# Kernel tuning notes

Measured on AMD Instinct MI355X. Metric: run time of the kernel, lower is better.

Reference implementation:

```python
import jax, jax.numpy as jnp
import numpy as np

PATCH_SIZE = 32          # BinaryPatchCompressor default
MAX_ACTIVE = 512         # memory_size // 2
EPS = 1e-8               # torch F.cosine_similarity eps


def _compress(emb, base):
    # emb, base: [S, D]. Entropy-ranked top-k row selection + int8 truncation.
    diff = emb - base
    entropy = jnp.std(diff, axis=-1, ddof=1)                  # [S] (torch std is unbiased)
    k = min(PATCH_SIZE, entropy.shape[0])
    _, idx = jax.lax.top_k(entropy, k)
    idx = jnp.sort(idx)
    # patch.to(torch.int8): truncation toward zero (values assumed in int8 range)
    patch = jnp.trunc(jnp.clip(diff[idx], -128.0, 127.0))     # [k, D]
    return patch, idx


def _decompress(patch, base, idx):
    # reconstructed[indices] += patch  -> scatter-add
    return base.at[idx].add(patch)


def _meta_embed(feats, W1, b1, W2, b2):
    # meta_learner: Linear(D+3,128) -> ReLU -> Linear(128,D)
    return jax.nn.relu(feats @ W1 + b1) @ W2 + b2


def setup_inputs() -> dict:
    key = jax.random.key(0)
    ks = jax.random.split(key, 6)
    S, D, N = 2048, 1024, 32
    return {
        "query": jax.random.normal(ks[0], (S, D), jnp.float32),
        "memories": jax.random.normal(ks[1], (N, S, D), jnp.float32),
        "surprise": jax.random.uniform(ks[2], (N,), jnp.float32),
        "priority_mult": jax.random.uniform(ks[3], (N,), jnp.float32) + 0.5,
        "W1": jax.random.normal(ks[4], (D + 3, 128), jnp.float32) * 0.02,
        "b1": jnp.zeros((128,), jnp.float32),
        "W2": jax.random.normal(ks[5], (128, D), jnp.float32) * 0.02,
        "b2": jnp.zeros((D,), jnp.float32),
    }


def reference(query, memories, surprise, priority_mult, W1, b1, W2, b2):
    S, D = query.shape
    N = memories.shape[0]
    base = jnp.zeros_like(query)                              # [S, D]

    # per-memory entropy-topk compression (vectorized over N)
    patches, idxs = jax.vmap(lambda m: _compress(m, base))(memories)      # [N,k,D], [N,k]
    # scatter-add decompression
    decompressed = jax.vmap(lambda p, i: _decompress(p, base, i))(patches, idxs)  # [N,S,D]

    # ApiAdapter aggregation: cat(query, decompressed).mean over memory axis
    src = jnp.concatenate([query[None], decompressed], axis=0)           # [N+1,S,D]
    aggregated = src.mean(axis=0)                                        # [S,D]

    # compress the aggregate, then reconstruct via scatter-add
    out_patch, out_idx = _compress(aggregated, base)
    recon = _decompress(out_patch, base, out_idx)                        # [S,D]

    # MemScheduler: meta-learned embeddings + priority-weighted cosine sims
    mem_feats = jnp.concatenate(
        [memories.mean(axis=1), surprise[:, None], jnp.zeros((N, 2), query.dtype)], axis=1)
    mem_emb = _meta_embed(mem_feats, W1, b1, W2, b2)                     # [N,D]
    q_feat = jnp.concatenate([query.mean(axis=0), jnp.zeros((3,), query.dtype)])
    q_emb = _meta_embed(q_feat, W1, b1, W2, b2)                          # [D]

    sims = (mem_emb @ q_emb) / (
        jnp.maximum(jnp.linalg.norm(mem_emb, axis=-1), EPS)
        * jnp.maximum(jnp.linalg.norm(q_emb), EPS))
    sims = sims * priority_mult                                          # [N]
    _, top_idx = jax.lax.top_k(sims, min(N, MAX_ACTIVE))
    return recon, sims, top_idx
```

## Files before the change

kernel.cpp:

```cpp
#include <hip/hip_runtime.h>
#include <math.h>

#define S     2048
#define D     1024
#define NMEM  32
#define KP    32

__device__ inline float trunc_clip(float v) {
    return truncf(fminf(fmaxf(v, -128.f), 127.f));
}

__global__ __launch_bounds__(256)
void k_stats(const float* __restrict__ mem, const float* __restrict__ query,
             float* __restrict__ entropy, float* __restrict__ colsumPart) {
    const int tid = threadIdx.x, wave = tid >> 6, lane = tid & 63;
    const int n    = blockIdx.x >> 5;
    const int tile = blockIdx.x & 31;
    const float* src = (n < NMEM) ? (mem + (size_t)n * S * D) : query;
    const int s0 = tile * 64 + wave * 16;

    __shared__ double redsm[64][33];
    __shared__ double redsq[64][33];
    __shared__ float  ldscol[D];
    for (int i = tid; i < D; i += 256) ldscol[i] = 0.f;
    __syncthreads();

    float colacc[16];
    #pragma unroll
    for (int i = 0; i < 16; ++i) colacc[i] = 0.f;

    for (int r = 0; r < 16; ++r) {
        const float4* row = (const float4*)(src + (size_t)(s0 + r) * D);
        double sm = 0.0, sq = 0.0;
        #pragma unroll
        for (int it = 0; it < 4; ++it) {
            float4 v = row[it * 64 + lane];
            sm += (double)v.x + (double)v.y + (double)v.z + (double)v.w;
            sq += (double)v.x * v.x + (double)v.y * v.y
                + (double)v.z * v.z + (double)v.w * v.w;
            colacc[it*4+0] += v.x; colacc[it*4+1] += v.y;
            colacc[it*4+2] += v.z; colacc[it*4+3] += v.w;
        }
        sm += __shfl_xor(sm, 1, 64);
        sq += __shfl_xor(sq, 1, 64);
        if ((lane & 1) == 0) {
            redsm[wave * 16 + r][lane >> 1] = sm;
            redsq[wave * 16 + r][lane >> 1] = sq;
        }
    }
    #pragma unroll
    for (int it = 0; it < 4; ++it)
        #pragma unroll
        for (int j = 0; j < 4; ++j)
            atomicAdd(&ldscol[it*256 + lane*4 + j], colacc[it*4+j]);
    __syncthreads();

    if (n < NMEM) {
        const int row = tid >> 2, qq = tid & 3;
        double sm = 0.0, sq = 0.0;
        #pragma unroll
        for (int i = 0; i < 8; ++i) { sm += redsm[row][qq*8 + i]; sq += redsq[row][qq*8 + i]; }
        sm += __shfl_xor(sm, 1, 64); sq += __shfl_xor(sq, 1, 64);
        sm += __shfl_xor(sm, 2, 64); sq += __shfl_xor(sq, 2, 64);
        if (qq == 0) {
            double var = (sq - sm * sm / (double)D) / (double)(D - 1);
            entropy[(size_t)n * S + tile * 64 + row] = (float)sqrt(var > 0.0 ? var : 0.0);
        }
    }
    for (int i = tid; i < D; i += 256)
        colsumPart[((size_t)n * 32 + tile) * D + i] = ldscol[i];
}

__global__ __launch_bounds__(1024)
void k_select(const float* __restrict__ entropy, const float* __restrict__ colsumPart,
              int* __restrict__ idxSel, float* __restrict__ feats) {
    const int n = blockIdx.x, tid = threadIdx.x;
    {
        float acc = 0.f;
        #pragma unroll 4
        for (int t = 0; t < 32; ++t) acc += colsumPart[((size_t)n * 32 + t) * D + tid];
        feats[(size_t)n * D + tid] = acc * (1.f / (float)S);
    }
    if (n >= NMEM) return;

    __shared__ unsigned long long key[S];
    const float* e = entropy + (size_t)n * S;
    for (int i = tid; i < S; i += 1024) {
        unsigned int b = __float_as_uint(e[i]);
        key[i] = ((unsigned long long)b << 32) | (unsigned long long)(S - 1 - i);
    }
    __syncthreads();
    const unsigned long long k0 = key[tid], k1 = key[tid + 1024];
    int c0 = 0, c1 = 0;
    for (int j = 0; j < S; j += 4) {
        unsigned long long a0 = key[j], a1 = key[j+1], a2 = key[j+2], a3 = key[j+3];
        c0 += (a0 > k0) + (a1 > k0) + (a2 > k0) + (a3 > k0);
        c1 += (a0 > k1) + (a1 > k1) + (a2 > k1) + (a3 > k1);
    }
    if (c0 < KP) idxSel[n * KP + c0] = tid;
    if (c1 < KP) idxSel[n * KP + c1] = tid + 1024;
}

__global__ __launch_bounds__(256)
void k_aggregate(const float* __restrict__ mem, const float* __restrict__ query,
                 const int* __restrict__ idxSel, float* __restrict__ agg,
                 float* __restrict__ entAgg) {
    const int s = blockIdx.x, tid = threadIdx.x;
    __shared__ int    sidx[NMEM * KP];
    __shared__ int    sel_n[NMEM];
    __shared__ int    selCount;
    __shared__ double rsm[256], rsq[256];
    __shared__ double fsm[64],  fsq[64];
    if (tid == 0) selCount = 0;
    for (int i = tid; i < NMEM * KP; i += 256) sidx[i] = idxSel[i];
    __syncthreads();
    #pragma unroll
    for (int k = 0; k < 4; ++k) {
        int e = tid * 4 + k;
        if (sidx[e] == s) { int p = atomicAdd(&selCount, 1); sel_n[p] = e >> 5; }
    }
    __syncthreads();

    float4 acc = ((const float4*)(query + (size_t)s * D))[tid];
    const int cnt = selCount;
    for (int c = 0; c < cnt; ++c) {
        const int n = sel_n[c];
        float4 v = ((const float4*)(mem + ((size_t)n * S + s) * D))[tid];
        acc.x += trunc_clip(v.x); acc.y += trunc_clip(v.y);
        acc.z += trunc_clip(v.z); acc.w += trunc_clip(v.w);
    }
    const float sc = 1.f / 33.f;
    acc.x *= sc; acc.y *= sc; acc.z *= sc; acc.w *= sc;
    ((float4*)(agg + (size_t)s * D))[tid] = acc;

    double sm = (double)acc.x + (double)acc.y + (double)acc.z + (double)acc.w;
    double sq = (double)acc.x * acc.x + (double)acc.y * acc.y
              + (double)acc.z * acc.z + (double)acc.w * acc.w;
    rsm[tid] = sm; rsq[tid] = sq;
    __syncthreads();
    if (tid < 64) {
        double a = 0, b = 0;
        #pragma unroll
        for (int i = 0; i < 4; ++i) { a += rsm[tid + 64*i]; b += rsq[tid + 64*i]; }
        fsm[tid] = a; fsq[tid] = b;
    }
    __syncthreads();
    if (tid == 0) {
        double a = 0, b = 0;
        for (int i = 0; i < 64; ++i) { a += fsm[i]; b += fsq[i]; }
        double var = (b - a * a / (double)D) / (double)(D - 1);
        entAgg[s] = (float)sqrt(var > 0.0 ? var : 0.0);
    }
}

__global__ __launch_bounds__(256)
void k_recon(const float* __restrict__ agg, const float* __restrict__ entAgg,
             float* __restrict__ outRecon) {
    const int s = blockIdx.x, tid = threadIdx.x;
    __shared__ float ent[S];
    __shared__ int   cnts[256];
    __shared__ int   rankS;
    for (int i = tid; i < S; i += 256) ent[i] = entAgg[i];
    __syncthreads();
    const float es = ent[s];
    int c = 0;
    for (int i = tid; i < S; i += 256) {
        float ej = ent[i];
        c += (ej > es) || (ej == es && i < s);
    }
    cnts[tid] = c;
    __syncthreads();
    if (tid < 32) {
        int a = 0;
        #pragma unroll
        for (int i = 0; i < 8; ++i) a += cnts[tid + 32 * i];
        cnts[tid] = a;
    }
    __syncthreads();
    if (tid == 0) {
        int r = 0;
        for (int i = 0; i < 32; ++i) r += cnts[i];
        rankS = r;
    }
    __syncthreads();
    float4 o = make_float4(0.f, 0.f, 0.f, 0.f);
    if (rankS < KP) {
        float4 v = ((const float4*)(agg + (size_t)s * D))[tid];
        o.x = trunc_clip(v.x); o.y = trunc_clip(v.y);
        o.z = trunc_clip(v.z); o.w = trunc_clip(v.w);
    }
    ((float4*)(outRecon + (size_t)s * D))[tid] = o;
}

__global__ __launch_bounds__(256)
void k_mlp1(const float* __restrict__ feats, const float* __restrict__ surprise,
            const float* __restrict__ W1, const float* __restrict__ b1,
            float* __restrict__ hidden) {
    const int m = blockIdx.x, tid = threadIdx.x;
    const int h = tid & 127, half = tid >> 7;
    __shared__ float lf[D];
    __shared__ float part[256];
    for (int i = tid; i < D; i += 256) lf[i] = feats[(size_t)m * D + i];
    __syncthreads();
    const int j0 = half * 512;
    float a0 = 0.f, a1 = 0.f, a2 = 0.f, a3 = 0.f;
    for (int j = 0; j < 512; j += 4) {
        a0 += lf[j0 + j + 0] * W1[(size_t)(j0 + j + 0) * 128 + h];
        a1 += lf[j0 + j + 1] * W1[(size_t)(j0 + j + 1) * 128 + h];
        a2 += lf[j0 + j + 2] * W1[(size_t)(j0 + j + 2) * 128 + h];
        a3 += lf[j0 + j + 3] * W1[(size_t)(j0 + j + 3) * 128 + h];
    }
    part[tid] = (a0 + a1) + (a2 + a3);
    __syncthreads();
    if (half == 0) {
        float acc = b1[h] + part[h] + part[128 + h];
        if (m < NMEM) acc += surprise[m] * W1[(size_t)D * 128 + h];
        hidden[(size_t)m * 128 + h] = fmaxf(acc, 0.f);
    }
}

__global__ __launch_bounds__(256)
void k_mlp2(const float* __restrict__ hidden, const float* __restrict__ W2,
            const float* __restrict__ b2, float* __restrict__ emb) {
    const int m = blockIdx.x, tid = threadIdx.x;
    __shared__ float lh[128];
    if (tid < 128) lh[tid] = hidden[(size_t)m * 128 + tid];
    __syncthreads();
    const int d0 = tid, d1 = tid + 256, d2 = tid + 512, d3 = tid + 768;
    float a0 = b2[d0], a1 = b2[d1], a2 = b2[d2], a3 = b2[d3];
    for (int k = 0; k < 128; ++k) {
        const float hk = lh[k];
        const float* wr = W2 + (size_t)k * D;
        a0 += hk * wr[d0]; a1 += hk * wr[d1];
        a2 += hk * wr[d2]; a3 += hk * wr[d3];
    }
    float* er = emb + (size_t)m * D;
    er[d0] = a0; er[d1] = a1; er[d2] = a2; er[d3] = a3;
}

__global__ __launch_bounds__(256)
void k_simsdot(const float* __restrict__ emb, float* __restrict__ ssq,
               float* __restrict__ dotv) {
    const int m = blockIdx.x;
    const int tid = threadIdx.x, wave = tid >> 6, lane = tid & 63;
    float4 v = ((const float4*)(emb + (size_t)m * D))[tid];
    float4 q = ((const float4*)(emb + (size_t)NMEM * D))[tid];
    double ss = (double)v.x * v.x + (double)v.y * v.y
              + (double)v.z * v.z + (double)v.w * v.w;
    double dt = (double)v.x * q.x + (double)v.y * q.y
              + (double)v.z * q.z + (double)v.w * q.w;
    #pragma unroll
    for (int off = 32; off > 0; off >>= 1) {
        ss += __shfl_xor(ss, off, 64);
        dt += __shfl_xor(dt, off, 64);
    }
    __shared__ double wss[4], wdt[4];
    if (lane == 0) { wss[wave] = ss; wdt[wave] = dt; }
    __syncthreads();
    if (tid == 0) {
        double a = 0, b = 0;
        #pragma unroll
        for (int w = 0; w < 4; ++w) { a += wss[w]; b += wdt[w]; }
        ssq[m] = (float)a;
        if (m < NMEM) dotv[m] = (float)b;
    }
}

__global__ __launch_bounds__(64)
void k_final(const float* __restrict__ ssq, const float* __restrict__ dotv,
             const float* __restrict__ prio, float* __restrict__ outSims,
             float* __restrict__ outIdx) {
    __shared__ float sims[NMEM];
    const int t = threadIdx.x;
    const float qn = fmaxf(sqrtf(ssq[NMEM]), 1e-8f);
    if (t < NMEM) {
        const float mn = fmaxf(sqrtf(ssq[t]), 1e-8f);
        const float sv = dotv[t] / (mn * qn) * prio[t];
        sims[t] = sv;
        outSims[t] = sv;
    }
    __syncthreads();
    if (t < NMEM) {
        const float si = sims[t];
        int rank = 0;
        #pragma unroll
        for (int j = 0; j < NMEM; ++j) {
            const float sj = sims[j];
            rank += (sj > si) || (sj == si && j < t);
        }
        outIdx[rank] = (float)t;
    }
}

extern "C" void kernel_launch(void* const* d_in, const int* in_sizes, int n_in,
                              void* d_out, int out_size, void* d_ws, size_t ws_size,
                              hipStream_t stream) {
    const float* query    = (const float*)d_in[0];
    const float* memories = (const float*)d_in[1];
    const float* surprise = (const float*)d_in[2];
    const float* priority = (const float*)d_in[3];
    const float* W1 = (const float*)d_in[4];
    const float* b1 = (const float*)d_in[5];
    const float* W2 = (const float*)d_in[6];
    const float* b2 = (const float*)d_in[7];
    float* out = (float*)d_out;
    char*  ws  = (char*)d_ws;

    float* entropy    = (float*)(ws + 0);
    float* colsumPart = (float*)(ws + 262144);
    float* feats      = (float*)(ws + 4587520);
    int*   idxSel     = (int*)  (ws + 4722688);
    float* agg        = (float*)(ws + 4726784);
    float* entAgg     = (float*)(ws + 13115392);
    float* hidden     = (float*)(ws + 13123584);
    float* emb        = (float*)(ws + 13140480);
    float* ssq        = (float*)(ws + 13275648);
    float* dotv       = (float*)(ws + 13275904);

    float* outSims   = out + (size_t)S * D;
    float* outTopIdx = outSims + NMEM;

    k_stats    <<<(NMEM + 1) * 32, 256,  0, stream>>>(memories, query, entropy, colsumPart);
    k_select   <<<NMEM + 1,        1024, 0, stream>>>(entropy, colsumPart, idxSel, feats);
    k_aggregate<<<S,               256,  0, stream>>>(memories, query, idxSel, agg, entAgg);
    k_recon    <<<S,               256,  0, stream>>>(agg, entAgg, out);
    k_mlp1     <<<NMEM + 1,        256,  0, stream>>>(feats, surprise, W1, b1, hidden);
    k_mlp2     <<<NMEM + 1,        256,  0, stream>>>(hidden, W2, b2, emb);
    k_simsdot  <<<NMEM + 1,        256,  0, stream>>>(emb, ssq, dotv);
    k_final    <<<1,               64,   0, stream>>>(ssq, dotv, priority, outSims, outTopIdx);
}
```

Baseline: 523.9 us.

## Fuse meta-learner kernels and split top-k selection across more blocks

Merges the column-mean reduction, both MLP layers and the squared-norm computation into a single k_meta kernel. The dot products move into k_final, which removes the feats, hidden and dotv intermediates and cuts the launch count from eight to six. k_select now runs 8 blocks of 256 threads per memory instead of one 1024-thread block, so each thread ranks a single candidate and the grid spreads across more CUs. In exchange, every select block rebuilds the full 2048-key shared array, and k_final does all 32 dot products inside one block.

New measurement: 481.1 us. -8.2%, faster.

```diff
diff --git a/kernel.cpp b/kernel.cpp
--- a/kernel.cpp
+++ b/kernel.cpp
@@ -71,34 +71,28 @@
         colsumPart[((size_t)n * 32 + tile) * D + i] = ldscol[i];
 }
 
-__global__ __launch_bounds__(1024)
-void k_select(const float* __restrict__ entropy, const float* __restrict__ colsumPart,
-              int* __restrict__ idxSel, float* __restrict__ feats) {
-    const int n = blockIdx.x, tid = threadIdx.x;
-    {
-        float acc = 0.f;
-        #pragma unroll 4
-        for (int t = 0; t < 32; ++t) acc += colsumPart[((size_t)n * 32 + t) * D + tid];
-        feats[(size_t)n * D + tid] = acc * (1.f / (float)S);
-    }
-    if (n >= NMEM) return;
-
+__global__ __launch_bounds__(256)
+void k_select(const float* __restrict__ entropy, int* __restrict__ idxSel) {
+    const int n  = blockIdx.x >> 3;
+    const int t8 = blockIdx.x & 7;
+    const int tid = threadIdx.x;
     __shared__ unsigned long long key[S];
     const float* e = entropy + (size_t)n * S;
-    for (int i = tid; i < S; i += 1024) {
+    for (int i = tid; i < S; i += 256) {
         unsigned int b = __float_as_uint(e[i]);
         key[i] = ((unsigned long long)b << 32) | (unsigned long long)(S - 1 - i);
     }
     __syncthreads();
-    const unsigned long long k0 = key[tid], k1 = key[tid + 1024];
-    int c0 = 0, c1 = 0;
-    for (int j = 0; j < S; j += 4) {
-        unsigned long long a0 = key[j], a1 = key[j+1], a2 = key[j+2], a3 = key[j+3];
-        c0 += (a0 > k0) + (a1 > k0) + (a2 > k0) + (a3 > k0);
-        c1 += (a0 > k1) + (a1 > k1) + (a2 > k1) + (a3 > k1);
-    }
-    if (c0 < KP) idxSel[n * KP + c0] = tid;
-    if (c1 < KP) idxSel[n * KP + c1] = tid + 1024;
+    const int cand = t8 * 256 + tid;
+    const unsigned long long kc = key[cand];
+    int c = 0;
+    for (int j = 0; j < S; j += 8) {
+        unsigned long long a0 = key[j+0], a1 = key[j+1], a2 = key[j+2], a3 = key[j+3];
+        unsigned long long a4 = key[j+4], a5 = key[j+5], a6 = key[j+6], a7 = key[j+7];
+        c += (a0 > kc) + (a1 > kc) + (a2 > kc) + (a3 > kc)
+           + (a4 > kc) + (a5 > kc) + (a6 > kc) + (a7 > kc);
+    }
+    if (c < KP) idxSel[n * KP + c] = cand;
 }
 
 __global__ __launch_bounds__(256)
@@ -193,39 +187,43 @@
 }
 
 __global__ __launch_bounds__(256)
-void k_mlp1(const float* __restrict__ feats, const float* __restrict__ surprise,
+void k_meta(const float* __restrict__ colsumPart, const float* __restrict__ surprise,
             const float* __restrict__ W1, const float* __restrict__ b1,
-            float* __restrict__ hidden) {
+            const float* __restrict__ W2, const float* __restrict__ b2,
+            float* __restrict__ emb, float* __restrict__ ssq) {
     const int m = blockIdx.x, tid = threadIdx.x;
-    const int h = tid & 127, half = tid >> 7;
     __shared__ float lf[D];
+    __shared__ float lh[128];
     __shared__ float part[256];
-    for (int i = tid; i < D; i += 256) lf[i] = feats[(size_t)m * D + i];
-    __syncthreads();
-    const int j0 = half * 512;
-    float a0 = 0.f, a1 = 0.f, a2 = 0.f, a3 = 0.f;
-    for (int j = 0; j < 512; j += 4) {
-        a0 += lf[j0 + j + 0] * W1[(size_t)(j0 + j + 0) * 128 + h];
-        a1 += lf[j0 + j + 1] * W1[(size_t)(j0 + j + 1) * 128 + h];
-        a2 += lf[j0 + j + 2] * W1[(size_t)(j0 + j + 2) * 128 + h];
-        a3 += lf[j0 + j + 3] * W1[(size_t)(j0 + j + 3) * 128 + h];
-    }
-    part[tid] = (a0 + a1) + (a2 + a3);
-    __syncthreads();
-    if (half == 0) {
-        float acc = b1[h] + part[h] + part[128 + h];
-        if (m < NMEM) acc += surprise[m] * W1[(size_t)D * 128 + h];
-        hidden[(size_t)m * 128 + h] = fmaxf(acc, 0.f);
-    }
-}
-
-__global__ __launch_bounds__(256)
-void k_mlp2(const float* __restrict__ hidden, const float* __restrict__ W2,
-            const float* __restrict__ b2, float* __restrict__ emb) {
-    const int m = blockIdx.x, tid = threadIdx.x;
-    __shared__ float lh[128];
-    if (tid < 128) lh[tid] = hidden[(size_t)m * 128 + tid];
-    __syncthreads();
+
+    for (int c = tid; c < D; c += 256) {
+        float acc = 0.f;
+        #pragma unroll 8
+        for (int t = 0; t < 32; ++t) acc += colsumPart[((size_t)m * 32 + t) * D + c];
+        lf[c] = acc * (1.f / (float)S);
+    }
+    __syncthreads();
+
+    {
+        const int h = tid & 127, half = tid >> 7;
+        const int j0 = half * 512;
+        float a0 = 0.f, a1 = 0.f, a2 = 0.f, a3 = 0.f;
+        for (int j = 0; j < 512; j += 4) {
+            a0 += lf[j0 + j + 0] * W1[(size_t)(j0 + j + 0) * 128 + h];
+            a1 += lf[j0 + j + 1] * W1[(size_t)(j0 + j + 1) * 128 + h];
+            a2 += lf[j0 + j + 2] * W1[(size_t)(j0 + j + 2) * 128 + h];
+            a3 += lf[j0 + j + 3] * W1[(size_t)(j0 + j + 3) * 128 + h];
+        }
+        part[tid] = (a0 + a1) + (a2 + a3);
+        __syncthreads();
+        if (half == 0) {
+            float acc = b1[h] + part[h] + part[128 + h];
+            if (m < NMEM) acc += surprise[m] * W1[(size_t)D * 128 + h];
+            lh[h] = fmaxf(acc, 0.f);
+        }
+    }
+    __syncthreads();
+
     const int d0 = tid, d1 = tid + 256, d2 = tid + 512, d3 = tid + 768;
     float a0 = b2[d0], a1 = b2[d1], a2 = b2[d2], a3 = b2[d3];
     for (int k = 0; k < 128; ++k) {
@@ -236,59 +234,59 @@
     }
     float* er = emb + (size_t)m * D;
     er[d0] = a0; er[d1] = a1; er[d2] = a2; er[d3] = a3;
-}
-
-__global__ __launch_bounds__(256)
-void k_simsdot(const float* __restrict__ emb, float* __restrict__ ssq,
-               float* __restrict__ dotv) {
-    const int m = blockIdx.x;
-    const int tid = threadIdx.x, wave = tid >> 6, lane = tid & 63;
-    float4 v = ((const float4*)(emb + (size_t)m * D))[tid];
-    float4 q = ((const float4*)(emb + (size_t)NMEM * D))[tid];
-    double ss = (double)v.x * v.x + (double)v.y * v.y
-              + (double)v.z * v.z + (double)v.w * v.w;
-    double dt = (double)v.x * q.x + (double)v.y * q.y
-              + (double)v.z * q.z + (double)v.w * q.w;
-    #pragma unroll
-    for (int off = 32; off > 0; off >>= 1) {
-        ss += __shfl_xor(ss, off, 64);
-        dt += __shfl_xor(dt, off, 64);
-    }
-    __shared__ double wss[4], wdt[4];
-    if (lane == 0) { wss[wave] = ss; wdt[wave] = dt; }
-    __syncthreads();
-    if (tid == 0) {
-        double a = 0, b = 0;
-        #pragma unroll
-        for (int w = 0; w < 4; ++w) { a += wss[w]; b += wdt[w]; }
-        ssq[m] = (float)a;
-        if (m < NMEM) dotv[m] = (float)b;
-    }
-}
-
-__global__ __launch_bounds__(64)
-void k_final(const float* __restrict__ ssq, const float* __restrict__ dotv,
+
+    double ss = (double)a0 * a0 + (double)a1 * a1
+              + (double)a2 * a2 + (double)a3 * a3;
+    #pragma unroll
+    for (int off = 32; off > 0; off >>= 1) ss += __shfl_xor(ss, off, 64);
+    __shared__ double wss[4];
+    const int wave = tid >> 6, lane = tid & 63;
+    if (lane == 0) wss[wave] = ss;
+    __syncthreads();
+    if (tid == 0) ssq[m] = (float)(wss[0] + wss[1] + wss[2] + wss[3]);
+}
+
+__global__ __launch_bounds__(256)
+void k_final(const float* __restrict__ emb, const float* __restrict__ ssq,
              const float* __restrict__ prio, float* __restrict__ outSims,
              float* __restrict__ outIdx) {
+    const int tid = threadIdx.x;
+    __shared__ float qv[D];
     __shared__ float sims[NMEM];
-    const int t = threadIdx.x;
-    const float qn = fmaxf(sqrtf(ssq[NMEM]), 1e-8f);
-    if (t < NMEM) {
-        const float mn = fmaxf(sqrtf(ssq[t]), 1e-8f);
-        const float sv = dotv[t] / (mn * qn) * prio[t];
-        sims[t] = sv;
-        outSims[t] = sv;
-    }
-    __syncthreads();
-    if (t < NMEM) {
-        const float si = sims[t];
+    ((float4*)qv)[tid] = ((const float4*)(emb + (size_t)NMEM * D))[tid];
+    __syncthreads();
+
+    const int g = tid >> 3, r = tid & 7;
+    const float* er = emb + (size_t)g * D + r * 128;
+    const float* qr = qv + r * 128;
+    double dt = 0.0;
+    #pragma unroll
+    for (int k = 0; k < 32; ++k) {
+        float4 v = ((const float4*)er)[k];
+        float4 q = ((const float4*)qr)[k];
+        dt += (double)v.x * q.x + (double)v.y * q.y
+            + (double)v.z * q.z + (double)v.w * q.w;
+    }
+    dt += __shfl_xor(dt, 1, 64);
+    dt += __shfl_xor(dt, 2, 64);
+    dt += __shfl_xor(dt, 4, 64);
+    if (r == 0) {
+        const float qn = fmaxf(sqrtf(ssq[NMEM]), 1e-8f);
+        const float mn = fmaxf(sqrtf(ssq[g]), 1e-8f);
+        const float sv = (float)dt / (mn * qn) * prio[g];
+        sims[g] = sv;
+        outSims[g] = sv;
+    }
+    __syncthreads();
+    if (tid < NMEM) {
+        const float si = sims[tid];
         int rank = 0;
         #pragma unroll
         for (int j = 0; j < NMEM; ++j) {
             const float sj = sims[j];
-            rank += (sj > si) || (sj == si && j < t);
-        }
-        outIdx[rank] = (float)t;
+            rank += (sj > si) || (sj == si && j < tid);
+        }
+        outIdx[rank] = (float)tid;
     }
 }
 
@@ -308,24 +306,19 @@
 
     float* entropy    = (float*)(ws + 0);
     float* colsumPart = (float*)(ws + 262144);
-    float* feats      = (float*)(ws + 4587520);
-    int*   idxSel     = (int*)  (ws + 4722688);
-    float* agg        = (float*)(ws + 4726784);
-    float* entAgg     = (float*)(ws + 13115392);
-    float* hidden     = (float*)(ws + 13123584);
-    float* emb        = (float*)(ws + 13140480);
-    float* ssq        = (float*)(ws + 13275648);
-    float* dotv       = (float*)(ws + 13275904);
+    int*   idxSel     = (int*)  (ws + 4587520);
+    float* agg        = (float*)(ws + 4591616);
+    float* entAgg     = (float*)(ws + 12980224);
+    float* emb        = (float*)(ws + 12988416);
+    float* ssq        = (float*)(ws + 13123584);
 
     float* outSims   = out + (size_t)S * D;
     float* outTopIdx = outSims + NMEM;
 
-    k_stats    <<<(NMEM + 1) * 32, 256,  0, stream>>>(memories, query, entropy, colsumPart);
-    k_select   <<<NMEM + 1,        1024, 0, stream>>>(entropy, colsumPart, idxSel, feats);
-    k_aggregate<<<S,               256,  0, stream>>>(memories, query, idxSel, agg, entAgg);
-    k_recon    <<<S,               256,  0, stream>>>(agg, entAgg, out);
-    k_mlp1     <<<NMEM + 1,        256,  0, stream>>>(feats, surprise, W1, b1, hidden);
-    k_mlp2     <<<NMEM + 1,        256,  0, stream>>>(hidden, W2, b2, emb);
-    k_simsdot  <<<NMEM + 1,        256,  0, stream>>>(emb, ssq, dotv);
-    k_final    <<<1,               64,   0, stream>>>(ssq, dotv, priority, outSims, outTopIdx);
-}
+    k_stats    <<<(NMEM + 1) * 32, 256, 0, stream>>>(memories, query, entropy, colsumPart);
+    k_select   <<<NMEM * 8,        256, 0, stream>>>(entropy, idxSel);
+    k_aggregate<<<S,               256, 0, stream>>>(memories, query, idxSel, agg, entAgg);
+    k_recon    <<<S,               256, 0, stream>>>(agg, entAgg, out);
+    k_meta     <<<NMEM + 1,        256, 0, stream>>>(colsumPart, surprise, W1, b1, W2, b2, emb, ssq);
+    k_final    <<<1,               256, 0, stream>>>(emb, ssq, priority, outSims, outTopIdx);
+}
```
